# Kernel optimization log

Hardware: AMD Instinct MI355X
Metric: run time of the kernel (lower is better)

The kernel has to match this reference:

```python
import jax, jax.numpy as jnp
from jax import lax
import numpy as np

GRID_SIZE = 5   # spline_points
DEGREE = 3      # spline_degree
NUM_BASES = GRID_SIZE + DEGREE  # 8 basis functions per input element


def make_grid():
    # efficient-kan style uniform grid on [-1, 1] extended by DEGREE knots each side
    h = 2.0 / GRID_SIZE
    return jnp.arange(-DEGREE, GRID_SIZE + DEGREE + 1, dtype=jnp.float32) * h - 1.0  # [G+2k+1]


def b_splines(x, grid, k):
    """Cox-de Boor B-spline bases. x: [N, F] -> [N, F, G+k]."""
    x = x[..., None]  # [N, F, 1]
    bases = ((x >= grid[:-1]) & (x < grid[1:])).astype(x.dtype)  # order 0
    for d in range(1, k + 1):
        left = (x - grid[:-(d + 1)]) / (grid[d:-1] - grid[:-(d + 1)])
        right = (grid[d + 1:] - x) / (grid[d + 1:] - grid[1:-d])
        bases = left * bases[..., :-1] + right * bases[..., 1:]
    return bases


def kan_conv(x, base_w, spline_w, ksize, pad, grid):
    """KANConv2d: unfold patches, apply KANLinear (silu base + spline term).
    x: [B, C, H, W]; base_w: [O, C*k*k]; spline_w: [O, C*k*k, NUM_BASES]."""
    patches = lax.conv_general_dilated_patches(
        x, (ksize, ksize), (1, 1), [(pad, pad), (pad, pad)])  # [B, C*k*k, Ho, Wo]
    B, F, Ho, Wo = patches.shape
    p = patches.transpose(0, 2, 3, 1).reshape(-1, F)  # [B*Ho*Wo, F]
    base = jax.nn.silu(p) @ base_w.T
    bs = b_splines(p, grid, DEGREE).reshape(p.shape[0], F * NUM_BASES)
    sp = bs @ spline_w.reshape(spline_w.shape[0], F * NUM_BASES).T
    out = base + sp  # [B*Ho*Wo, O]
    return out.reshape(B, Ho, Wo, -1).transpose(0, 3, 1, 2)


def maxpool2(x):
    return lax.reduce_window(x, -jnp.inf, lax.max, (1, 1, 2, 2), (1, 1, 2, 2), 'VALID')


def setup_inputs() -> dict:
    key = jax.random.key(0)
    ks = jax.random.split(key, 12)
    def w(k, shape, fan_in):
        return jax.random.normal(k, shape, dtype=jnp.float32) / np.sqrt(fan_in)
    B = 2048
    return {
        'x': jax.random.normal(ks[0], (B, 1, 28, 28), dtype=jnp.float32),
        'base_w1': w(ks[1], (4, 1 * 9), 9),
        'spline_w1': w(ks[2], (4, 1 * 9, NUM_BASES), 9 * NUM_BASES) * 0.1,
        'base_w2': w(ks[3], (8, 4 * 9), 36),
        'spline_w2': w(ks[4], (8, 4 * 9, NUM_BASES), 36 * NUM_BASES) * 0.1,
        'base_w3': w(ks[5], (16, 8 * 9), 72),
        'spline_w3': w(ks[6], (16, 8 * 9, NUM_BASES), 72 * NUM_BASES) * 0.1,
        'base_w4': w(ks[7], (32, 16 * 4), 64),
        'spline_w4': w(ks[8], (32, 16 * 4, NUM_BASES), 64 * NUM_BASES) * 0.1,
        'fc_w': w(ks[9], (10, 32), 32),
        'fc_b': jnp.zeros((10,), dtype=jnp.float32),
    }


def reference(x, base_w1, spline_w1, base_w2, spline_w2, base_w3, spline_w3,
              base_w4, spline_w4, fc_w, fc_b):
    grid = make_grid()
    h = kan_conv(x, base_w1, spline_w1, 3, 1, grid)   # [B,4,28,28]
    h = maxpool2(h)                                   # [B,4,14,14]
    h = kan_conv(h, base_w2, spline_w2, 3, 1, grid)   # [B,8,14,14]
    h = maxpool2(h)                                   # [B,8,7,7]
    h = kan_conv(h, base_w3, spline_w3, 3, 1, grid)   # [B,16,7,7]
    h = maxpool2(h)                                   # [B,16,3,3]
    h = kan_conv(h, base_w4, spline_w4, 2, 1, grid)   # [B,32,4,4]
    h = jnp.mean(h, axis=(2, 3))                      # global avg pool -> [B,32]
    return h @ fc_w.T + fc_b                          # [B,10]
```

## Files before the change

kernel.cpp:

```cpp
#include <hip/hip_runtime.h>

#define DEV __device__ __forceinline__

typedef __fp16 h8 __attribute__((ext_vector_type(8)));
typedef float f32x4 __attribute__((ext_vector_type(4)));
union U4H { uint4 u; h8 h; };
union HS { _Float16 h; unsigned short s; };

DEV unsigned short h16(float x) { HS z; z.h = (_Float16)x; return z.s; }
DEV float silu_f(float v) { return v / (1.0f + __expf(-v)); }

DEV void bspline8(float x, float bb[8]) {
    float b[11];
#pragma unroll
    for (int i = 0; i < 11; ++i) {
        float g0 = (i - 3) * 0.4f - 1.0f;
        float g1 = (i - 2) * 0.4f - 1.0f;
        b[i] = ((x >= g0) && (x < g1)) ? 1.0f : 0.0f;
    }
#pragma unroll
    for (int d = 1; d <= 3; ++d) {
        const float inv = 1.0f / (0.4f * (float)d);
#pragma unroll
        for (int i = 0; i < 11 - d; ++i) {
            float gl = (i - 3) * 0.4f - 1.0f;
            float gr = (i - 3 + d + 1) * 0.4f - 1.0f;
            b[i] = (x - gl) * inv * b[i] + (gr - x) * inv * b[i + 1];
        }
    }
#pragma unroll
    for (int j = 0; j < 8; ++j) bb[j] = b[j];
}

template <int CIN, int H, int W, int STRIDE>
DEV void expand(const float* src, char* planes, int tid) {
    constexpr int WC = W + 2, HC = H + 2;
    constexpr int CELLS = CIN * HC * WC;
    for (int cell = tid; cell < CELLS; cell += 256) {
        int c = cell / (HC * WC);
        int rr = cell - c * (HC * WC);
        int row = rr / WC, col = rr - row * WC;
        int y = row - 1, x = col - 1;
        bool inb = ((unsigned)y < (unsigned)H) && ((unsigned)x < (unsigned)W);
        float v = inb ? src[c * H * W + y * W + x] : 0.0f;
        float sil = silu_f(v);
        float shf = (float)(_Float16)sil;
        unsigned sh = h16(sil);
        unsigned slo = h16(sil - shf);
        char* rec = planes + (size_t)(c * (HC * STRIDE) + row * STRIDE + col) * 32;
        uint4 r0; r0.x = sh;          r0.y = 0u; r0.z = 0u; r0.w = 0u;
        uint4 r1; r1.x = (slo << 16); r1.y = sh; r1.z = 0u; r1.w = 0u;
        *(uint4*)rec = r0;
        *(uint4*)(rec + 16) = r1;
        float u = (v + 2.2f) * 2.5f;
        if (u >= 0.0f && u < 11.0f) {
            int mi = (int)u;
            float t = u - (float)mi;
            float t2 = t * t, t3 = t2 * t;
            float omt = 1.0f - t;
            float p3 = omt * omt * omt * (1.0f / 6.0f);
            float p2 = (3.0f * t3 - 6.0f * t2 + 4.0f) * (1.0f / 6.0f);
            float p1 = (-3.0f * t3 + 3.0f * t2 + 3.0f * t + 1.0f) * (1.0f / 6.0f);
            float p0 = t3 * (1.0f / 6.0f);
            int s0 = mi - 3;
            _Float16* bp = (_Float16*)(rec + 2);
            if (s0 >= 0) bp[s0] = (_Float16)p3;
            if (s0 >= -1 && s0 <= 6) bp[s0 + 1] = (_Float16)p2;
            if (s0 >= -2 && s0 <= 5) bp[s0 + 2] = (_Float16)p1;
            if (s0 <= 4) bp[s0 + 3] = (_Float16)p0;
        }
    }
}

template <int H, int STRIDE>
DEV constexpr int tapoff(int t) {
    return ((t / 9) * ((H + 2) * STRIDE) + ((t % 9) / 3) * STRIDE + (t % 9) % 3) * 32;
}

template <int O, int PHV, int PWV>
DEV void poolwrite(f32x4 acc, int ty, int tx, int ln, float* s_next) {
    const int n = ln & 15, q = ln >> 4;
    float q0 = fmaxf(acc[0], acc[1]);
    float q1 = fmaxf(acc[2], acc[3]);
    float r0 = fmaxf(q0, __shfl_xor(q0, 32));
    float r1 = fmaxf(q1, __shfl_xor(q1, 32));
    if (ln < 32 && n < O && ty < PHV) {
        int ppx = tx * 4 + (q & 1) * 2;
        float* dst = s_next + n * (PHV * PWV) + ty * PWV + ppx;
        if (ppx < PWV) dst[0] = r0;
        if (ppx + 1 < PWV) dst[1] = r1;
    }
}

template <int CIN, int H, int W, int O, int STRIDE, int NT, int KC, int BWC,
          int TX, int TPW, int PHV, int PWV>
DEV void layer_mfma(const uint4* __restrict__ pwB, const char* planes,
                    float* s_next, int tid) {
    const int wv = tid >> 6, ln = tid & 63;
    const int m = ln & 15;
    const int half = ln >> 4;
    const int tapsel = (half >> 1) & 1;
    const int bh = (half & 1) << 4;

    if constexpr (KC == BWC) {
        uint4 bw[BWC];
#pragma unroll
        for (int i = 0; i < BWC; ++i) bw[i] = pwB[i * 64 + ln];
#pragma unroll
        for (int tt = 0; tt < TPW; ++tt) {
            const int gid = wv * TPW + tt;
            const int ty = gid / TX, tx = gid - ty * TX;
            const int py = min(2 * ty + (m >> 3), H - 1);
            const int px = min(tx * 8 + (m & 7), W - 1);
            const int base = (py * STRIDE + px) * 32 + bh;
            f32x4 acc = {0.f, 0.f, 0.f, 0.f};
#pragma unroll
            for (int i = 0; i < BWC; ++i) {
                const int t0 = min(2 * i, NT - 1), t1 = min(2 * i + 1, NT - 1);
                const int off = tapsel ? tapoff<H, STRIDE>(t1) : tapoff<H, STRIDE>(t0);
                U4H a; a.u = *(const uint4*)(planes + base + off);
                U4H b; b.u = bw[i];
                acc = __builtin_amdgcn_mfma_f32_16x16x32_f16(a.h, b.h, acc, 0, 0, 0);
            }
            poolwrite<O, PHV, PWV>(acc, ty, tx, ln, s_next);
        }
    } else {
        f32x4 acc[TPW];
        int base[TPW], tyA[TPW], txA[TPW];
#pragma unroll
        for (int tt = 0; tt < TPW; ++tt) {
            acc[tt] = {0.f, 0.f, 0.f, 0.f};
            const int gid = wv * TPW + tt;
            tyA[tt] = gid / TX;
            txA[tt] = gid - tyA[tt] * TX;
            const int py = min(2 * tyA[tt] + (m >> 3), H - 1);
            const int px = min(txA[tt] * 8 + (m & 7), W - 1);
            base[tt] = (py * STRIDE + px) * 32 + bh;
        }
#pragma unroll
        for (int kc = 0; kc < KC; kc += BWC) {
            uint4 bw[BWC];
#pragma unroll
            for (int i = 0; i < BWC; ++i) bw[i] = pwB[(kc + i) * 64 + ln];
#pragma unroll
            for (int i = 0; i < BWC; ++i) {
                const int kf = kc + i;
                const int t0 = min(2 * kf, NT - 1), t1 = min(2 * kf + 1, NT - 1);
                const int off = tapsel ? tapoff<H, STRIDE>(t1) : tapoff<H, STRIDE>(t0);
#pragma unroll
                for (int tt = 0; tt < TPW; ++tt) {
                    U4H a; a.u = *(const uint4*)(planes + base[tt] + off);
                    U4H b; b.u = bw[i];
                    acc[tt] = __builtin_amdgcn_mfma_f32_16x16x32_f16(a.h, b.h, acc[tt], 0, 0, 0);
                }
            }
        }
#pragma unroll
        for (int tt = 0; tt < TPW; ++tt)
            poolwrite<O, PHV, PWV>(acc[tt], tyA[tt], txA[tt], ln, s_next);
    }
}

DEV float wval(const float* wb, const float* ws, int NT, int O, int n, int k) {
    int tap = k >> 4, comp = k & 15;
    if (n >= O || tap >= NT) return 0.f;
    if (comp >= 1 && comp <= 8) return ws[(n * NT + tap) * 8 + comp - 1];
    if (comp > 10) return 0.f;
    float w = wb[n * NT + tap];
    float hi = (float)(_Float16)w;
    return (comp == 10) ? (w - hi) : hi;
}

DEV unsigned packw(float a, float b) {
    return (unsigned)h16(a) | ((unsigned)h16(b) << 16);
}

__global__ __launch_bounds__(256) void kan_prep(
    const float* __restrict__ wb1, const float* __restrict__ ws1,
    const float* __restrict__ wb2, const float* __restrict__ ws2,
    const float* __restrict__ wb3, const float* __restrict__ ws3,
    const float* __restrict__ wb4, const float* __restrict__ ws4,
    float* __restrict__ wsbase) {
    float* wr = wsbase;
    const int bid = blockIdx.x;
    const int tid = threadIdx.x;

    if (bid == 0) {
        for (int i = tid; i < 512; i += 256) {
            int o = i / 16, c = i % 16;
            float s = 0.0f;
#pragma unroll
            for (int q = 0; q < 4; ++q) s += wb4[o * 64 + c * 4 + q];
            wr[i] = s;
        }
    } else if (bid == 1) {
        __shared__ float zb[8];
        if (tid == 0) {
            float zbb[8];
            bspline8(0.0f, zbb);
#pragma unroll
            for (int j = 0; j < 8; ++j) zb[j] = zbb[j];
        }
        __syncthreads();
        const int o = tid >> 3, j = tid & 7;
        float s = 0.0f;
        for (int f = 0; f < 64; ++f) s += ws4[(o * 64 + f) * 8 + j];
        s *= zb[j];
        s += __shfl_xor(s, 1);
        s += __shfl_xor(s, 2);
        s += __shfl_xor(s, 4);
        if (j == 0) wr[4608 + o] = 7.0f * s;
    } else if (bid < 18) {
        const int i = (bid - 2) * 256 + tid;
        int j = i % 8, c = (i / 8) % 16, o = i / 128;
        float s = 0.0f;
#pragma unroll
        for (int q = 0; q < 4; ++q) s += ws4[(o * 64 + c * 4 + q) * 8 + j];
        wr[512 + i] = s;
    } else {
        int g = (bid - 18) * 256 + tid;
        if (g < 15104) {
            const float *wb, *ws;
            unsigned* dst;
            int NT, O, rel;
            if (g < 1280) {
                wb = wb1; ws = ws1; NT = 9; O = 4; rel = g;
                dst = (unsigned*)(wsbase + 4640);
            } else if (g < 5888) {
                wb = wb2; ws = ws2; NT = 36; O = 8; rel = g - 1280;
                dst = (unsigned*)(wsbase + 5920);
            } else {
                wb = wb3; ws = ws3; NT = 72; O = 16; rel = g - 5888;
                dst = (unsigned*)(wsbase + 10528);
            }
            int kf = rel >> 8;
            int lane = (rel >> 2) & 63;
            int j = rel & 3;
            int k0 = kf * 32 + ((lane >> 4) & 3) * 8 + j * 2;
            int n = lane & 15;
            dst[rel] = packw(wval(wb, ws, NT, O, n, k0),
                             wval(wb, ws, NT, O, n, k0 + 1));
        }
    }
}

__global__ __launch_bounds__(256, 4) void kan_fused(
    const float* __restrict__ x, const float* __restrict__ wsbase,
    const float* __restrict__ fcw, const float* __restrict__ fcb,
    float* __restrict__ out) {
    __shared__ uint4 s_planes4[2176];
    __shared__ float s_next[784];
    __shared__ float s_sum[144];
    __shared__ float s_pool[32];
    char* planes = (char*)s_planes4;

    const int b = blockIdx.x;
    const int tid = threadIdx.x;
    const float* wr = wsbase;
    const uint4* pw1 = (const uint4*)(wsbase + 4640);
    const uint4* pw2 = (const uint4*)(wsbase + 5920);
    const uint4* pw3 = (const uint4*)(wsbase + 10528);

    expand<1, 28, 28, 31>(x + (size_t)b * 784, planes, tid);
    __syncthreads();
    layer_mfma<1, 28, 28, 4, 31, 9, 5, 5, 4, 14, 14, 14>(pw1, planes, s_next, tid);
    __syncthreads();

    expand<4, 14, 14, 17>(s_next, planes, tid);
    __syncthreads();
    layer_mfma<4, 14, 14, 8, 17, 36, 18, 9, 2, 4, 7, 7>(pw2, planes, s_next, tid);
    __syncthreads();

    expand<8, 7, 7, 9>(s_next, planes, tid);
    __syncthreads();
    layer_mfma<8, 7, 7, 16, 9, 72, 36, 9, 1, 1, 3, 3>(pw3, planes, s_next, tid);
    __syncthreads();

    float* s_exp = (float*)s_planes4;
    if (tid < 144) {
        float v = s_next[tid];
        float bb[8];
        bspline8(v, bb);
        s_exp[tid * 9 + 0] = silu_f(v);
#pragma unroll
        for (int j = 0; j < 8; ++j) s_exp[tid * 9 + 1 + j] = bb[j];
    }
    __syncthreads();
    if (tid < 144) {
        int c = tid / 9, comp = tid - (tid / 9) * 9;
        float s = 0.0f;
#pragma unroll
        for (int p = 0; p < 9; ++p) s += s_exp[(c * 9 + p) * 9 + comp];
        s_sum[tid] = s;
    }
    __syncthreads();
    if (tid < 32) {
        int o = tid;
        float acc = wr[4608 + o];
        for (int c = 0; c < 16; ++c) {
            acc += wr[o * 16 + c] * s_sum[c * 9 + 0];
#pragma unroll
            for (int j = 0; j < 8; ++j)
                acc += wr[512 + (o * 16 + c) * 8 + j] * s_sum[c * 9 + 1 + j];
        }
        s_pool[o] = acc * (1.0f / 16.0f);
    }
    __syncthreads();
    if (tid < 10) {
        float acc = fcb[tid];
#pragma unroll
        for (int c = 0; c < 32; ++c) acc += fcw[tid * 32 + c] * s_pool[c];
        out[(size_t)b * 10 + tid] = acc;
    }
}

extern "C" void kernel_launch(void* const* d_in, const int* in_sizes, int n_in,
                              void* d_out, int out_size, void* d_ws, size_t ws_size,
                              hipStream_t stream) {
    const float* x = (const float*)d_in[0];
    const float* wb1 = (const float*)d_in[1];
    const float* ws1 = (const float*)d_in[2];
    const float* wb2 = (const float*)d_in[3];
    const float* ws2 = (const float*)d_in[4];
    const float* wb3 = (const float*)d_in[5];
    const float* ws3 = (const float*)d_in[6];
    const float* wb4 = (const float*)d_in[7];
    const float* ws4 = (const float*)d_in[8];
    const float* fcw = (const float*)d_in[9];
    const float* fcb = (const float*)d_in[10];
    float* out = (float*)d_out;

    const int B = in_sizes[0] / (28 * 28);
    float* wsbase = (float*)d_ws;

    kan_prep<<<77, 256, 0, stream>>>(wb1, ws1, wb2, ws2, wb3, ws3, wb4, ws4,
                                     wsbase);
    kan_fused<<<B, 256, 0, stream>>>(x, wsbase, fcw, fcb, out);
}
```

Measured before the change: 56.72 us.

## Split expanded records into two dense 16-byte planes and write full records

The expand stage now builds each cell's full 32-byte feature record in registers (silu hi/lo plus the 8 spline bases) and stores it as two dense uint4 writes into separate low and high planes. Previously it zero-filled the record and then did scattered 2-byte basis writes into a padded stride layout. Removing the padding shrinks LDS from 2176 to 2048 uint4 and makes address math a simple cell*16 offset. This trades the partial stores for extra register work to select the four nonzero bases, and it changes the LDS bank pattern of the MFMA A-operand loads.

```diff
diff --git a/kernel.cpp b/kernel.cpp
--- a/kernel.cpp
+++ b/kernel.cpp
@@ -7,8 +7,10 @@
 union U4H { uint4 u; h8 h; };
 union HS { _Float16 h; unsigned short s; };
 
-DEV unsigned short h16(float x) { HS z; z.h = (_Float16)x; return z.s; }
+DEV unsigned h16(float x) { HS z; z.h = (_Float16)x; return (unsigned)z.s; }
 DEV float silu_f(float v) { return v / (1.0f + __expf(-v)); }
+
+#define PLANE_OFF 16384
 
 DEV void bspline8(float x, float bb[8]) {
     float b[11];
@@ -32,7 +34,7 @@
     for (int j = 0; j < 8; ++j) bb[j] = b[j];
 }
 
-template <int CIN, int H, int W, int STRIDE>
+template <int CIN, int H, int W>
 DEV void expand(const float* src, char* planes, int tid) {
     constexpr int WC = W + 2, HC = H + 2;
     constexpr int CELLS = CIN * HC * WC;
@@ -45,36 +47,41 @@
         float v = inb ? src[c * H * W + y * W + x] : 0.0f;
         float sil = silu_f(v);
         float shf = (float)(_Float16)sil;
+        float slo = sil - shf;
+        float u = (v + 2.2f) * 2.5f;
+        int mi = (int)u;
+        int s0 = (u >= 0.0f && u < 11.0f) ? (mi - 3) : -100;
+        float t = u - (float)mi;
+        float t2 = t * t, t3 = t2 * t;
+        float omt = 1.0f - t;
+        float p3 = omt * omt * omt * (1.0f / 6.0f);
+        float p2 = (3.0f * t3 - 6.0f * t2 + 4.0f) * (1.0f / 6.0f);
+        float p1 = (-3.0f * t3 + 3.0f * t2 + 3.0f * t + 1.0f) * (1.0f / 6.0f);
+        float p0 = t3 * (1.0f / 6.0f);
+        float B[8];
+#pragma unroll
+        for (int j = 0; j < 8; ++j) {
+            int d = j - s0;
+            B[j] = (d == 0) ? p3 : (d == 1) ? p2 : (d == 2) ? p1 : (d == 3) ? p0 : 0.0f;
+        }
         unsigned sh = h16(sil);
-        unsigned slo = h16(sil - shf);
-        char* rec = planes + (size_t)(c * (HC * STRIDE) + row * STRIDE + col) * 32;
-        uint4 r0; r0.x = sh;          r0.y = 0u; r0.z = 0u; r0.w = 0u;
-        uint4 r1; r1.x = (slo << 16); r1.y = sh; r1.z = 0u; r1.w = 0u;
-        *(uint4*)rec = r0;
-        *(uint4*)(rec + 16) = r1;
-        float u = (v + 2.2f) * 2.5f;
-        if (u >= 0.0f && u < 11.0f) {
-            int mi = (int)u;
-            float t = u - (float)mi;
-            float t2 = t * t, t3 = t2 * t;
-            float omt = 1.0f - t;
-            float p3 = omt * omt * omt * (1.0f / 6.0f);
-            float p2 = (3.0f * t3 - 6.0f * t2 + 4.0f) * (1.0f / 6.0f);
-            float p1 = (-3.0f * t3 + 3.0f * t2 + 3.0f * t + 1.0f) * (1.0f / 6.0f);
-            float p0 = t3 * (1.0f / 6.0f);
-            int s0 = mi - 3;
-            _Float16* bp = (_Float16*)(rec + 2);
-            if (s0 >= 0) bp[s0] = (_Float16)p3;
-            if (s0 >= -1 && s0 <= 6) bp[s0 + 1] = (_Float16)p2;
-            if (s0 >= -2 && s0 <= 5) bp[s0 + 2] = (_Float16)p1;
-            if (s0 <= 4) bp[s0 + 3] = (_Float16)p0;
-        }
-    }
-}
-
-template <int H, int STRIDE>
-DEV constexpr int tapoff(int t) {
-    return ((t / 9) * ((H + 2) * STRIDE) + ((t % 9) / 3) * STRIDE + (t % 9) % 3) * 32;
+        uint4 lo, hi;
+        lo.x = sh | (h16(B[0]) << 16);
+        lo.y = h16(B[1]) | (h16(B[2]) << 16);
+        lo.z = h16(B[3]) | (h16(B[4]) << 16);
+        lo.w = h16(B[5]) | (h16(B[6]) << 16);
+        hi.x = h16(B[7]) | (h16(slo) << 16);
+        hi.y = sh;
+        hi.z = 0u;
+        hi.w = 0u;
+        *(uint4*)(planes + (size_t)cell * 16) = lo;
+        *(uint4*)(planes + PLANE_OFF + (size_t)cell * 16) = hi;
+    }
+}
+
+template <int HC, int SC>
+DEV constexpr int tapcell(int t) {
+    return (t / 9) * (HC * SC) + ((t % 9) / 3) * SC + (t % 9) % 3;
 }
 
 template <int O, int PHV, int PWV>
@@ -92,15 +99,16 @@
     }
 }
 
-template <int CIN, int H, int W, int O, int STRIDE, int NT, int KC, int BWC,
-          int TX, int TPW, int PHV, int PWV>
+template <int CIN, int H, int W, int O, int NT, int KC, int BWC, int TX,
+          int TPW, int PHV, int PWV>
 DEV void layer_mfma(const uint4* __restrict__ pwB, const char* planes,
                     float* s_next, int tid) {
+    constexpr int HC = H + 2, SC = W + 2;
     const int wv = tid >> 6, ln = tid & 63;
     const int m = ln & 15;
     const int half = ln >> 4;
     const int tapsel = (half >> 1) & 1;
-    const int bh = (half & 1) << 4;
+    const int psel = (half & 1) ? PLANE_OFF : 0;
 
     if constexpr (KC == BWC) {
         uint4 bw[BWC];
@@ -112,12 +120,13 @@
             const int ty = gid / TX, tx = gid - ty * TX;
             const int py = min(2 * ty + (m >> 3), H - 1);
             const int px = min(tx * 8 + (m & 7), W - 1);
-            const int base = (py * STRIDE + px) * 32 + bh;
+            const int base = ((py + 1) * SC + (px + 1)) * 16 + psel;
             f32x4 acc = {0.f, 0.f, 0.f, 0.f};
 #pragma unroll
             for (int i = 0; i < BWC; ++i) {
                 const int t0 = min(2 * i, NT - 1), t1 = min(2 * i + 1, NT - 1);
-                const int off = tapsel ? tapoff<H, STRIDE>(t1) : tapoff<H, STRIDE>(t0);
+                const int off =
+                    (tapsel ? tapcell<HC, SC>(t1) : tapcell<HC, SC>(t0)) * 16 - SC * 16 - 16;
                 U4H a; a.u = *(const uint4*)(planes + base + off);
                 U4H b; b.u = bw[i];
                 acc = __builtin_amdgcn_mfma_f32_16x16x32_f16(a.h, b.h, acc, 0, 0, 0);
@@ -135,7 +144,7 @@
             txA[tt] = gid - tyA[tt] * TX;
             const int py = min(2 * tyA[tt] + (m >> 3), H - 1);
             const int px = min(txA[tt] * 8 + (m & 7), W - 1);
-            base[tt] = (py * STRIDE + px) * 32 + bh;
+            base[tt] = ((py + 1) * SC + (px + 1)) * 16 + psel;
         }
 #pragma unroll
         for (int kc = 0; kc < KC; kc += BWC) {
@@ -146,7 +155,8 @@
             for (int i = 0; i < BWC; ++i) {
                 const int kf = kc + i;
                 const int t0 = min(2 * kf, NT - 1), t1 = min(2 * kf + 1, NT - 1);
-                const int off = tapsel ? tapoff<H, STRIDE>(t1) : tapoff<H, STRIDE>(t0);
+                const int off =
+                    (tapsel ? tapcell<HC, SC>(t1) : tapcell<HC, SC>(t0)) * 16 - SC * 16 - 16;
 #pragma unroll
                 for (int tt = 0; tt < TPW; ++tt) {
                     U4H a; a.u = *(const uint4*)(planes + base[tt] + off);
@@ -171,9 +181,7 @@
     return (comp == 10) ? (w - hi) : hi;
 }
 
-DEV unsigned packw(float a, float b) {
-    return (unsigned)h16(a) | ((unsigned)h16(b) << 16);
-}
+DEV unsigned packw(float a, float b) { return h16(a) | (h16(b) << 16); }
 
 __global__ __launch_bounds__(256) void kan_prep(
     const float* __restrict__ wb1, const float* __restrict__ ws1,
@@ -248,7 +256,7 @@
     const float* __restrict__ x, const float* __restrict__ wsbase,
     const float* __restrict__ fcw, const float* __restrict__ fcb,
     float* __restrict__ out) {
-    __shared__ uint4 s_planes4[2176];
+    __shared__ uint4 s_planes4[2048];
     __shared__ float s_next[784];
     __shared__ float s_sum[144];
     __shared__ float s_pool[32];
@@ -261,19 +269,19 @@
     const uint4* pw2 = (const uint4*)(wsbase + 5920);
     const uint4* pw3 = (const uint4*)(wsbase + 10528);
 
-    expand<1, 28, 28, 31>(x + (size_t)b * 784, planes, tid);
-    __syncthreads();
-    layer_mfma<1, 28, 28, 4, 31, 9, 5, 5, 4, 14, 14, 14>(pw1, planes, s_next, tid);
-    __syncthreads();
-
-    expand<4, 14, 14, 17>(s_next, planes, tid);
-    __syncthreads();
-    layer_mfma<4, 14, 14, 8, 17, 36, 18, 9, 2, 4, 7, 7>(pw2, planes, s_next, tid);
-    __syncthreads();
-
-    expand<8, 7, 7, 9>(s_next, planes, tid);
-    __syncthreads();
-    layer_mfma<8, 7, 7, 16, 9, 72, 36, 9, 1, 1, 3, 3>(pw3, planes, s_next, tid);
+    expand<1, 28, 28>(x + (size_t)b * 784, planes, tid);
+    __syncthreads();
+    layer_mfma<1, 28, 28, 4, 9, 5, 5, 4, 14, 14, 14>(pw1, planes, s_next, tid);
+    __syncthreads();
+
+    expand<4, 14, 14>(s_next, planes, tid);
+    __syncthreads();
+    layer_mfma<4, 14, 14, 8, 36, 18, 9, 2, 4, 7, 7>(pw2, planes, s_next, tid);
+    __syncthreads();
+
+    expand<8, 7, 7>(s_next, planes, tid);
+    __syncthreads();
+    layer_mfma<8, 7, 7, 16, 72, 36, 9, 1, 1, 3, 3>(pw3, planes, s_next, tid);
     __syncthreads();
 
     float* s_exp = (float*)s_planes4;
```

Result: slower. 70.64 us (+24.5%).
